# Kernel tuning notes

Hardware: AMD Instinct MI355X
Metric: run time of the kernel (lower is better)

## Reference

```python
import jax, jax.numpy as jnp
import numpy as np

W_BIT, OUT_F, IN_F, K = 4, 4096, 4096, 16
B, S = 4, 2048


def setup_inputs() -> dict:
    key = jax.random.key(0)
    k1, k2, k3, k4 = jax.random.split(key, 4)
    x = jax.random.normal(k1, (B, S, IN_F), dtype=jnp.float16)
    # bit-packed signs: 8 signs per byte, stored as int32 in [0, 256)
    qweight = jax.random.randint(k2, (W_BIT, OUT_F * IN_F // 8), 0, 256, dtype=jnp.int32)
    u = jax.random.normal(k3, (W_BIT, OUT_F, K), dtype=jnp.float16) * jnp.float16(0.1)
    vt = jax.random.normal(k4, (W_BIT, K, IN_F), dtype=jnp.float16) * jnp.float16(0.1)
    return {"x": x, "qweight": qweight, "u": u, "vt": vt}


def _unpack_sign(qweight, out_f, in_f, dtype):
    # [w_bit, N/8] packed bytes -> [w_bit, out_f, in_f] signs in {-1, +1}
    bits = (qweight[:, :, None] >> jnp.arange(8, dtype=qweight.dtype)) & 1
    sign = (2 * bits - 1).reshape(qweight.shape[0], out_f, in_f)
    return sign.astype(dtype)


def reference(x, qweight, u, vt):
    w_bit, out_f, _ = u.shape
    in_f = vt.shape[2]
    sign = _unpack_sign(qweight, out_f, in_f, u.dtype)          # [w_bit, out, in]
    lowrank = jnp.einsum('bok,bki->boi', u, vt)                  # per-bit u @ vt
    w = jnp.sum(sign * lowrank, axis=0)                          # [out, in]
    return x @ w.T                                               # [B, S, out]
```

## Files before the change

### kernel.cpp

```cpp
#include <hip/hip_runtime.h>
#include <stdint.h>


#define W_BITS 4
#define OUT_F  4096
#define IN_F   4096
#define K_RANK 16
#define M_TOT  8192
#define QW_PER_BIT (OUT_F * IN_F / 8)

typedef __attribute__((ext_vector_type(8))) short bf16x8;
typedef __attribute__((ext_vector_type(4))) float f32x4;

__device__ __forceinline__ unsigned short f2bf(float f) {
  union { float f; unsigned int u; } c; c.f = f;
  unsigned int r = c.u + 0x7fffu + ((c.u >> 16) & 1u);
  return (unsigned short)(r >> 16);
}

__global__ __launch_bounds__(256) void convert_x(
    const float* __restrict__ X, unsigned short* __restrict__ Xb, int n8)
{
  const int stride = gridDim.x * blockDim.x;
  for (int i = blockIdx.x * blockDim.x + threadIdx.x; i < n8; i += stride) {
    const f32x4 a = *reinterpret_cast<const f32x4*>(X + (size_t)i * 8);
    const f32x4 b = *reinterpret_cast<const f32x4*>(X + (size_t)i * 8 + 4);
    unsigned short o8[8] = {f2bf(a[0]), f2bf(a[1]), f2bf(a[2]), f2bf(a[3]),
                            f2bf(b[0]), f2bf(b[1]), f2bf(b[2]), f2bf(b[3])};
    *reinterpret_cast<uint4*>(Xb + (size_t)i * 8) = *reinterpret_cast<const uint4*>(o8);
  }
}

#define TO 4

__global__ __launch_bounds__(256) void build_w(
    const int*   __restrict__ qw,
    const float* __restrict__ u,
    const float* __restrict__ vt,
    unsigned short* __restrict__ w)
{
  const int tid = blockIdx.x * 256 + threadIdx.x;
  const int ig  = tid & 511;
  const int i0  = ig << 3;
  const int ob  = (tid >> 9) << 2;

  float acc[TO][8];
  #pragma unroll
  for (int t = 0; t < TO; ++t)
    #pragma unroll
    for (int ii = 0; ii < 8; ++ii) acc[t][ii] = 0.0f;

  #pragma unroll
  for (int bit = 0; bit < W_BITS; ++bit) {
    float lr[TO][8];
    #pragma unroll
    for (int t = 0; t < TO; ++t)
      #pragma unroll
      for (int ii = 0; ii < 8; ++ii) lr[t][ii] = 0.0f;

    const float* vbase = vt + (size_t)(bit * K_RANK) * IN_F + i0;
    const float* ubase = u + (size_t)(bit * OUT_F + ob) * K_RANK;

    #pragma unroll
    for (int k = 0; k < K_RANK; ++k) {
      const f32x4 v0 = *reinterpret_cast<const f32x4*>(vbase + (size_t)k * IN_F);
      const f32x4 v1 = *reinterpret_cast<const f32x4*>(vbase + (size_t)k * IN_F + 4);
      float vf[8] = {v0[0], v0[1], v0[2], v0[3], v1[0], v1[1], v1[2], v1[3]};
      #pragma unroll
      for (int t = 0; t < TO; ++t) {
        const float uk = ubase[t * K_RANK + k];
        #pragma unroll
        for (int ii = 0; ii < 8; ++ii) lr[t][ii] += uk * vf[ii];
      }
    }

    #pragma unroll
    for (int t = 0; t < TO; ++t) {
      const int q = qw[(size_t)bit * QW_PER_BIT + (size_t)(ob + t) * (IN_F / 8) + ig];
      #pragma unroll
      for (int ii = 0; ii < 8; ++ii)
        acc[t][ii] += ((q >> ii) & 1) ? lr[t][ii] : -lr[t][ii];
    }
  }

  #pragma unroll
  for (int t = 0; t < TO; ++t) {
    unsigned short o8[8];
    #pragma unroll
    for (int ii = 0; ii < 8; ++ii) o8[ii] = f2bf(acc[t][ii]);
    *reinterpret_cast<uint4*>(w + (size_t)(ob + t) * IN_F + i0) =
        *reinterpret_cast<const uint4*>(o8);
  }
}

__device__ __forceinline__ void gll16(unsigned short* lds, const unsigned short* g) {
  __builtin_amdgcn_global_load_lds(
      (const __attribute__((address_space(1))) unsigned int*)g,
      (__attribute__((address_space(3))) unsigned int*)lds,
      16, 0, 0);
}

__global__ __launch_bounds__(512, 2) void gemm_256(
    const unsigned short* __restrict__ X,
    const unsigned short* __restrict__ W,
    float* __restrict__ out)
{
  __shared__ __align__(16) unsigned short Al[2][256][64];
  __shared__ __align__(16) unsigned short Bl[2][256][64];

  const int bid = blockIdx.x;
  const int swz = (bid & 7) * 64 + (bid >> 3);
  const int bm = swz >> 4;
  const int bn = swz & 15;

  const int tid  = threadIdx.x;
  const int lane = tid & 63;
  const int wid  = tid >> 6;
  const int wm   = wid >> 2;
  const int wn   = wid & 3;

  const int sr = tid >> 3;
  const int sc = (((tid & 7) ^ (sr & 7)) << 3);

  const unsigned short* Abase = X + (size_t)(bm * 256 + sr) * IN_F + sc;
  const unsigned short* Bbase = W + (size_t)(bn * 256 + sr) * IN_F + sc;
  unsigned short* Alt = &Al[0][0][0] + tid * 8;
  unsigned short* Blt = &Bl[0][0][0] + tid * 8;

  const int fr  = lane & 15;
  const int sw0 = (((lane >> 4) ^ (fr & 7)) << 3);
  const int aRow = (wm * 16 + fr) * 64;
  const int bRow = (wn * 16 + fr) * 64;
  const unsigned short* Ar = &Al[0][0][0];
  const unsigned short* Br = &Bl[0][0][0];

  f32x4 acc[8][4];
  #pragma unroll
  for (int f = 0; f < 8; ++f)
    #pragma unroll
    for (int g = 0; g < 4; ++g)
      acc[f][g] = (f32x4){0.f, 0.f, 0.f, 0.f};

#define STAGE(buf, h, tn_) do {                                                        \
    const unsigned short* gs_ = ((h) < 2 ? Abase : Bbase)                              \
        + (size_t)(((h) & 1) * 128) * IN_F + (size_t)(tn_) * 64;                       \
    unsigned short* ld_ = ((h) < 2 ? Alt : Blt) + (buf) * 16384 + ((h) & 1) * 8192;    \
    gll16(ld_, gs_);                                                                   \
    gll16(ld_ + 4096, gs_ + (size_t)64 * IN_F);                                        \
  } while (0)

#define WAITBAR() do {                                                                 \
    asm volatile("s_waitcnt vmcnt(4)" ::: "memory");                                   \
    __builtin_amdgcn_s_barrier();                                                      \
    __builtin_amdgcn_sched_barrier(0);                                                 \
  } while (0)

#define PH_READ_A(mh_) {                                                               \
    _Pragma("unroll") for (int f = 0; f < 4; ++f)                                      \
      _Pragma("unroll") for (int ks = 0; ks < 2; ++ks)                                 \
        aF[f][ks] = *reinterpret_cast<const bf16x8*>(                                  \
            Ar + cbase + ((mh_) * 4 + f) * 2048 + aRow + ((ks * 32) ^ sw0)); }

#define PH_READ_B(nh_, dst_) {                                                         \
    _Pragma("unroll") for (int g = 0; g < 2; ++g)                                      \
      _Pragma("unroll") for (int ks = 0; ks < 2; ++ks)                                 \
        dst_[g][ks] = *reinterpret_cast<const bf16x8*>(                                \
            Br + cbase + ((nh_) * 2 + g) * 4096 + bRow + ((ks * 32) ^ sw0)); }

#define PH_MFMA(mh_, nh_, bsrc_) do {                                                  \
    __builtin_amdgcn_s_setprio(1);                                                     \
    _Pragma("unroll") for (int f = 0; f < 4; ++f)                                      \
      _Pragma("unroll") for (int g = 0; g < 2; ++g)                                    \
        _Pragma("unroll") for (int ks = 0; ks < 2; ++ks)                               \
          acc[(mh_) * 4 + f][(nh_) * 2 + g] = __builtin_amdgcn_mfma_f32_16x16x32_bf16( \
              aF[f][ks], bsrc_[g][ks], acc[(mh_) * 4 + f][(nh_) * 2 + g], 0, 0, 0);    \
    __builtin_amdgcn_s_setprio(0);                                                     \
  } while (0)

  STAGE(0, 0, 0);
  STAGE(0, 2, 0);
  STAGE(0, 3, 0);
  STAGE(0, 1, 0);
  asm volatile("s_waitcnt vmcnt(4)" ::: "memory");
  __builtin_amdgcn_s_barrier();
  __builtin_amdgcn_sched_barrier(0);

  bf16x8 aF[4][2], bF0[2][2], bF1[2][2];

  #pragma unroll 2
  for (int T = 0; T < 64; ++T) {
    const int cc = T & 1, oo = cc ^ 1;
    const int tn = (T < 63) ? T + 1 : 63;
    const int cbase = cc * 16384;

    PH_READ_A(0); PH_READ_B(0, bF0);
    STAGE(oo, 0, tn);
    WAITBAR();
    PH_MFMA(0, 0, bF0);
    __builtin_amdgcn_s_barrier();

    PH_READ_B(1, bF1);
    STAGE(oo, 2, tn);
    WAITBAR();
    PH_MFMA(0, 1, bF1);
    __builtin_amdgcn_s_barrier();

    PH_READ_A(1);
    STAGE(oo, 3, tn);
    WAITBAR();
    PH_MFMA(1, 1, bF1);
    __builtin_amdgcn_s_barrier();

    STAGE(oo, 1, tn);
    WAITBAR();
    PH_MFMA(1, 0, bF0);
    __builtin_amdgcn_s_barrier();
  }

  asm volatile("s_waitcnt vmcnt(0)" ::: "memory");

  const int rsub = (lane >> 4) << 2;
  #pragma unroll
  for (int f = 0; f < 8; ++f) {
    const int row = bm * 256 + (f * 2 + wm) * 16 + rsub;
    #pragma unroll
    for (int g = 0; g < 4; ++g) {
      const int col = bn * 256 + (g * 4 + wn) * 16 + (lane & 15);
      float* op = out + (size_t)row * OUT_F + col;
      #pragma unroll
      for (int j = 0; j < 4; ++j) op[(size_t)j * OUT_F] = acc[f][g][j];
    }
  }
#undef STAGE
#undef WAITBAR
#undef PH_READ_A
#undef PH_READ_B
#undef PH_MFMA
}

#define BM 128
#define BN 128
#define BK 32

__device__ __forceinline__ uint4 cvt8(f32x4 a, f32x4 b) {
  unsigned short o8[8] = {f2bf(a[0]), f2bf(a[1]), f2bf(a[2]), f2bf(a[3]),
                          f2bf(b[0]), f2bf(b[1]), f2bf(b[2]), f2bf(b[3])};
  return *reinterpret_cast<const uint4*>(o8);
}

__global__ __launch_bounds__(256) void gemm_f32stage(
    const float* __restrict__ X,
    const unsigned short* __restrict__ W,
    float* __restrict__ out)
{
  __shared__ __align__(16) unsigned short As[BM * BK];
  __shared__ __align__(16) unsigned short Bs[BN * BK];

  const int nbn = OUT_F / BN;
  const int cpx = (M_TOT / BM) * nbn / 8;
  const int bid = blockIdx.x;
  const int swz = (bid & 7) * cpx + (bid >> 3);
  const int bm = swz / nbn;
  const int bn = swz % nbn;

  const int tid  = threadIdx.x;
  const int lane = tid & 63;
  const int wid  = tid >> 6;
  const int wm   = wid >> 1;
  const int wn   = wid & 1;
  const int srow = tid >> 2;
  const int scol = (tid & 3) << 3;

  const float*          Ag = X + (size_t)(bm * BM + srow) * IN_F + scol;
  const unsigned short* Bg = W + (size_t)(bn * BN + srow) * IN_F + scol;

  const int fr = lane & 15;
  const int fk = (lane >> 4) << 3;

  f32x4 acc[4][4];
  #pragma unroll
  for (int m = 0; m < 4; ++m)
    #pragma unroll
    for (int n = 0; n < 4; ++n)
      acc[m][n] = (f32x4){0.f, 0.f, 0.f, 0.f};

  for (int k0 = 0; k0 < IN_F; k0 += BK) {
    const f32x4 a0a = *reinterpret_cast<const f32x4*>(Ag + k0);
    const f32x4 a0b = *reinterpret_cast<const f32x4*>(Ag + k0 + 4);
    const f32x4 a1a = *reinterpret_cast<const f32x4*>(Ag + (size_t)64 * IN_F + k0);
    const f32x4 a1b = *reinterpret_cast<const f32x4*>(Ag + (size_t)64 * IN_F + k0 + 4);
    const uint4 b0  = *reinterpret_cast<const uint4*>(Bg + k0);
    const uint4 b1  = *reinterpret_cast<const uint4*>(Bg + (size_t)64 * IN_F + k0);

    __syncthreads();
    *reinterpret_cast<uint4*>(As + tid * 8)        = cvt8(a0a, a0b);
    *reinterpret_cast<uint4*>(As + 2048 + tid * 8) = cvt8(a1a, a1b);
    *reinterpret_cast<uint4*>(Bs + tid * 8)        = b0;
    *reinterpret_cast<uint4*>(Bs + 2048 + tid * 8) = b1;
    __syncthreads();

    bf16x8 af[4], bfv[4];
    #pragma unroll
    for (int m = 0; m < 4; ++m)
      af[m] = *reinterpret_cast<const bf16x8*>(&As[(wm * 64 + m * 16 + fr) * BK + fk]);
    #pragma unroll
    for (int n = 0; n < 4; ++n)
      bfv[n] = *reinterpret_cast<const bf16x8*>(&Bs[(wn * 64 + n * 16 + fr) * BK + fk]);

    #pragma unroll
    for (int m = 0; m < 4; ++m)
      #pragma unroll
      for (int n = 0; n < 4; ++n)
        acc[m][n] = __builtin_amdgcn_mfma_f32_16x16x32_bf16(af[m], bfv[n], acc[m][n], 0, 0, 0);
  }

  const int rsub = (lane >> 4) << 2;
  #pragma unroll
  for (int m = 0; m < 4; ++m) {
    #pragma unroll
    for (int n = 0; n < 4; ++n) {
      const int col = bn * BN + wn * 64 + n * 16 + (lane & 15);
      #pragma unroll
      for (int j = 0; j < 4; ++j) {
        const int row = bm * BM + wm * 64 + m * 16 + rsub + j;
        out[(size_t)row * OUT_F + col] = acc[m][n][j];
      }
    }
  }
}

extern "C" void kernel_launch(void* const* d_in, const int* in_sizes, int n_in,
                              void* d_out, int out_size, void* d_ws, size_t ws_size,
                              hipStream_t stream) {
  (void)in_sizes; (void)n_in; (void)out_size;

  const float* x  = (const float*)d_in[0];
  const int*   qw = (const int*)d_in[1];
  const float* u  = (const float*)d_in[2];
  const float* vt = (const float*)d_in[3];
  float* out = (float*)d_out;

  unsigned short* w = (unsigned short*)d_ws;
  const size_t W_BYTES  = (size_t)OUT_F * IN_F * 2;
  const size_t XB_BYTES = (size_t)M_TOT * IN_F * 2;

  build_w<<<dim3(2048), dim3(256), 0, stream>>>(qw, u, vt, w);

  if (ws_size >= W_BYTES + XB_BYTES) {
    unsigned short* xb = w + (size_t)OUT_F * IN_F;
    convert_x<<<dim3(2048), dim3(256), 0, stream>>>(x, xb, M_TOT * IN_F / 8);
    gemm_256<<<dim3(512), dim3(512), 0, stream>>>(xb, w, out);
  } else {
    gemm_f32stage<<<dim3(2048), dim3(256), 0, stream>>>(x, w, out);
  }
}
```

Baseline: 365.7 us.

## Interleave LDS fragment reads with MFMAs in software-pipelined GEMM main loop

Restructures the bf16 GEMM main loop so LDS fragment reads for the next phase, and for the next K-tile, are issued between MFMA groups instead of in separate read phases before compute. Manual sched_barriers and explicit lgkmcnt waits control the ordering, and A/B fragments for the first tile are preloaded before the loop. The loop is unrolled by two with swapped register roles. This aims to hide LDS latency behind matrix-core work, at the cost of tighter hand scheduling and possible register pressure or hazards on buffer reuse.

```diff
diff --git a/kernel.cpp b/kernel.cpp
--- a/kernel.cpp
+++ b/kernel.cpp
@@ -155,26 +155,80 @@
     __builtin_amdgcn_sched_barrier(0);                                                 \
   } while (0)
 
-#define PH_READ_A(mh_) {                                                               \
-    _Pragma("unroll") for (int f = 0; f < 4; ++f)                                      \
-      _Pragma("unroll") for (int ks = 0; ks < 2; ++ks)                                 \
-        aF[f][ks] = *reinterpret_cast<const bf16x8*>(                                  \
-            Ar + cbase + ((mh_) * 4 + f) * 2048 + aRow + ((ks * 32) ^ sw0)); }
-
-#define PH_READ_B(nh_, dst_) {                                                         \
-    _Pragma("unroll") for (int g = 0; g < 2; ++g)                                      \
-      _Pragma("unroll") for (int ks = 0; ks < 2; ++ks)                                 \
-        dst_[g][ks] = *reinterpret_cast<const bf16x8*>(                                \
-            Br + cbase + ((nh_) * 2 + g) * 4096 + bRow + ((ks * 32) ^ sw0)); }
-
-#define PH_MFMA(mh_, nh_, bsrc_) do {                                                  \
+#define LGKMW(n_) do {                                                                 \
+    asm volatile("s_waitcnt lgkmcnt(" #n_ ")" ::: "memory");                           \
+    __builtin_amdgcn_sched_barrier(0);                                                 \
+  } while (0)
+
+#define SB() __builtin_amdgcn_sched_barrier(0)
+
+#define ENDPH() do {                                                                   \
+    __builtin_amdgcn_sched_barrier(0);                                                 \
+    __builtin_amdgcn_s_barrier();                                                      \
+  } while (0)
+
+#define RD_A(base_, mh_, f_, ks_)                                                      \
+    aF[f_][ks_] = *reinterpret_cast<const bf16x8*>(                                    \
+        Ar + (base_) + ((mh_) * 4 + (f_)) * 2048 + aRow + (((ks_) * 32) ^ sw0))
+
+#define RD_B(dst_, base_, nh_, g_, ks_)                                                \
+    dst_[g_][ks_] = *reinterpret_cast<const bf16x8*>(                                  \
+        Br + (base_) + ((nh_) * 2 + (g_)) * 4096 + bRow + (((ks_) * 32) ^ sw0))
+
+#define MF(mh_, nh_, f_, g_, ks_, bsrc_)                                               \
+    acc[(mh_) * 4 + (f_)][(nh_) * 2 + (g_)] = __builtin_amdgcn_mfma_f32_16x16x32_bf16( \
+        aF[f_][ks_], bsrc_[g_][ks_], acc[(mh_) * 4 + (f_)][(nh_) * 2 + (g_)], 0, 0, 0)
+
+#define MF4(mh_, nh_, f_, bsrc_) do {                                                  \
+    MF(mh_, nh_, f_, 0, 0, bsrc_); MF(mh_, nh_, f_, 0, 1, bsrc_);                      \
+    MF(mh_, nh_, f_, 1, 0, bsrc_); MF(mh_, nh_, f_, 1, 1, bsrc_); } while (0)
+
+#define KTILE(P_, Q_, CC_, OO_, tn_) do {                                              \
+    const int cb_ = (CC_) * 16384, ob_ = (OO_) * 16384;                                \
+                       \
+    STAGE(OO_, 2, tn_);                                                                \
+    WAITBAR();                                                                         \
+    LGKMW(0);                                                                          \
     __builtin_amdgcn_s_setprio(1);                                                     \
-    _Pragma("unroll") for (int f = 0; f < 4; ++f)                                      \
-      _Pragma("unroll") for (int g = 0; g < 2; ++g)                                    \
-        _Pragma("unroll") for (int ks = 0; ks < 2; ++ks)                               \
-          acc[(mh_) * 4 + f][(nh_) * 2 + g] = __builtin_amdgcn_mfma_f32_16x16x32_bf16( \
-              aF[f][ks], bsrc_[g][ks], acc[(mh_) * 4 + f][(nh_) * 2 + g], 0, 0, 0);    \
+    RD_B(Q_, cb_, 1, 0, 0); SB(); MF4(0, 0, 0, P_); SB();                              \
+    RD_B(Q_, cb_, 1, 0, 1); SB(); MF4(0, 0, 1, P_); SB();                              \
+    RD_B(Q_, cb_, 1, 1, 0); SB(); MF4(0, 0, 2, P_); SB();                              \
+    RD_B(Q_, cb_, 1, 1, 1); SB(); MF4(0, 0, 3, P_);                                    \
     __builtin_amdgcn_s_setprio(0);                                                     \
+    ENDPH();                                                                           \
+                        \
+    STAGE(OO_, 0, tn_);                                                                \
+    WAITBAR();                                                                         \
+    LGKMW(0);                                                                          \
+    __builtin_amdgcn_s_setprio(1);                                                     \
+    MF4(0, 1, 0, Q_); SB(); RD_A(cb_, 1, 0, 0); RD_A(cb_, 1, 0, 1); SB();              \
+    MF4(0, 1, 1, Q_); SB(); RD_A(cb_, 1, 1, 0); RD_A(cb_, 1, 1, 1); SB();              \
+    MF4(0, 1, 2, Q_); SB(); RD_A(cb_, 1, 2, 0); RD_A(cb_, 1, 2, 1); SB();              \
+    MF4(0, 1, 3, Q_); SB(); RD_A(cb_, 1, 3, 0); RD_A(cb_, 1, 3, 1);                    \
+    __builtin_amdgcn_s_setprio(0);                                                     \
+    ENDPH();                                                                           \
+                \
+    STAGE(OO_, 3, tn_);                                                                \
+    WAITBAR();                                                                         \
+    LGKMW(0);                                                                          \
+    __builtin_amdgcn_s_setprio(1);                                                     \
+    MF4(1, 1, 0, Q_); MF4(1, 1, 1, Q_); MF4(1, 1, 2, Q_); MF4(1, 1, 3, Q_);            \
+    __builtin_amdgcn_s_setprio(0);                                                     \
+    SB();                                                                              \
+    RD_B(Q_, ob_, 0, 0, 0); RD_B(Q_, ob_, 0, 0, 1);                                    \
+    RD_B(Q_, ob_, 0, 1, 0); RD_B(Q_, ob_, 0, 1, 1);                                    \
+    ENDPH();                                                                           \
+                  \
+    STAGE(OO_, 1, tn_);                                                                \
+    WAITBAR();                                                                         \
+    LGKMW(4);                                                                          \
+    __builtin_amdgcn_s_setprio(1);                                                     \
+    MF4(1, 0, 0, P_); SB(); RD_A(ob_, 0, 0, 0); RD_A(ob_, 0, 0, 1); SB();              \
+    MF4(1, 0, 1, P_); SB(); RD_A(ob_, 0, 1, 0); RD_A(ob_, 0, 1, 1); SB();              \
+    MF4(1, 0, 2, P_); SB(); RD_A(ob_, 0, 2, 0); RD_A(ob_, 0, 2, 1); SB();              \
+    MF4(1, 0, 3, P_); SB(); RD_A(ob_, 0, 3, 0); RD_A(ob_, 0, 3, 1);                    \
+    __builtin_amdgcn_s_setprio(0);                                                     \
+    ENDPH();                                                                           \
   } while (0)
 
   STAGE(0, 0, 0);
@@ -186,38 +240,23 @@
   __builtin_amdgcn_sched_barrier(0);
 
   bf16x8 aF[4][2], bF0[2][2], bF1[2][2];
-
-  #pragma unroll 2
-  for (int T = 0; T < 64; ++T) {
-    const int cc = T & 1, oo = cc ^ 1;
-    const int tn = (T < 63) ? T + 1 : 63;
-    const int cbase = cc * 16384;
-
-    PH_READ_A(0); PH_READ_B(0, bF0);
-    STAGE(oo, 0, tn);
-    WAITBAR();
-    PH_MFMA(0, 0, bF0);
-    __builtin_amdgcn_s_barrier();
-
-    PH_READ_B(1, bF1);
-    STAGE(oo, 2, tn);
-    WAITBAR();
-    PH_MFMA(0, 1, bF1);
-    __builtin_amdgcn_s_barrier();
-
-    PH_READ_A(1);
-    STAGE(oo, 3, tn);
-    WAITBAR();
-    PH_MFMA(1, 1, bF1);
-    __builtin_amdgcn_s_barrier();
-
-    STAGE(oo, 1, tn);
-    WAITBAR();
-    PH_MFMA(1, 0, bF0);
-    __builtin_amdgcn_s_barrier();
-  }
-
-  asm volatile("s_waitcnt vmcnt(0)" ::: "memory");
+  RD_A(0, 0, 0, 0); RD_A(0, 0, 0, 1);
+  RD_A(0, 0, 1, 0); RD_A(0, 0, 1, 1);
+  RD_A(0, 0, 2, 0); RD_A(0, 0, 2, 1);
+  RD_A(0, 0, 3, 0); RD_A(0, 0, 3, 1);
+  RD_B(bF0, 0, 0, 0, 0); RD_B(bF0, 0, 0, 0, 1);
+  RD_B(bF0, 0, 0, 1, 0); RD_B(bF0, 0, 0, 1, 1);
+
+  #pragma unroll 1
+  for (int Th = 0; Th < 32; ++Th) {
+    const int T0 = 2 * Th;
+    const int tnA = T0 + 1;
+    const int tnB = (T0 + 2 < 64) ? T0 + 2 : 63;
+    KTILE(bF0, bF1, 0, 1, tnA);
+    KTILE(bF1, bF0, 1, 0, tnB);
+  }
+
+  asm volatile("s_waitcnt vmcnt(0) lgkmcnt(0)" ::: "memory");
 
   const int rsub = (lane >> 4) << 2;
   #pragma unroll
@@ -233,9 +272,14 @@
   }
 #undef STAGE
 #undef WAITBAR
-#undef PH_READ_A
-#undef PH_READ_B
-#undef PH_MFMA
+#undef LGKMW
+#undef SB
+#undef ENDPH
+#undef RD_A
+#undef RD_B
+#undef MF
+#undef MF4
+#undef KTILE
 }
 
 #define BM 128
```

Result: no change. 367.6 us (+0.5%).

## Restructure GEMM main loop to one barrier per tile with batched LDS reads

Applied to the files above, without the earlier changes.

The bf16 GEMM K-loop is rescheduled. Each iteration now waits for all global-to-LDS loads and does a single barrier, then issues all four staging loads for the next tile up front. LDS fragment reads are batched and gated by lgkmcnt waits instead of four barrier-separated phases. This cuts barrier count and lets LDS reads overlap MFMAs, but the full vmcnt(0) wait at the start of each iteration may expose more global-load latency than the old partial vmcnt(4) waits.

```diff
diff --git a/kernel.cpp b/kernel.cpp
--- a/kernel.cpp
+++ b/kernel.cpp
@@ -149,31 +149,35 @@
     gll16(ld_ + 4096, gs_ + (size_t)64 * IN_F);                                        \
   } while (0)
 
-#define WAITBAR() do {                                                                 \
-    asm volatile("s_waitcnt vmcnt(4)" ::: "memory");                                   \
-    __builtin_amdgcn_s_barrier();                                                      \
+#define LGKMW(n_) do {                                                                 \
+    asm volatile("s_waitcnt lgkmcnt(" #n_ ")" ::: "memory");                           \
     __builtin_amdgcn_sched_barrier(0);                                                 \
   } while (0)
 
-#define PH_READ_A(mh_) {                                                               \
-    _Pragma("unroll") for (int f = 0; f < 4; ++f)                                      \
-      _Pragma("unroll") for (int ks = 0; ks < 2; ++ks)                                 \
-        aF[f][ks] = *reinterpret_cast<const bf16x8*>(                                  \
-            Ar + cbase + ((mh_) * 4 + f) * 2048 + aRow + ((ks * 32) ^ sw0)); }
-
-#define PH_READ_B(nh_, dst_) {                                                         \
-    _Pragma("unroll") for (int g = 0; g < 2; ++g)                                      \
-      _Pragma("unroll") for (int ks = 0; ks < 2; ++ks)                                 \
-        dst_[g][ks] = *reinterpret_cast<const bf16x8*>(                                \
-            Br + cbase + ((nh_) * 2 + g) * 4096 + bRow + ((ks * 32) ^ sw0)); }
-
-#define PH_MFMA(mh_, nh_, bsrc_) do {                                                  \
+#define SB() __builtin_amdgcn_sched_barrier(0)
+
+#define RD_A(base_, mh_, f_, ks_)                                                      \
+    aF[f_][ks_] = *reinterpret_cast<const bf16x8*>(                                    \
+        Ar + (base_) + ((mh_) * 4 + (f_)) * 2048 + aRow + (((ks_) * 32) ^ sw0))
+
+#define RD_B(dst_, base_, nh_, g_, ks_)                                                \
+    dst_[g_][ks_] = *reinterpret_cast<const bf16x8*>(                                  \
+        Br + (base_) + ((nh_) * 2 + (g_)) * 4096 + bRow + (((ks_) * 32) ^ sw0))
+
+#define MF(mh_, nh_, f_, g_, ks_, bsrc_)                                               \
+    acc[(mh_) * 4 + (f_)][(nh_) * 2 + (g_)] = __builtin_amdgcn_mfma_f32_16x16x32_bf16( \
+        aF[f_][ks_], bsrc_[g_][ks_], acc[(mh_) * 4 + (f_)][(nh_) * 2 + (g_)], 0, 0, 0)
+
+#define MF16(mh_, nh_, bsrc_) do {                                                     \
     __builtin_amdgcn_s_setprio(1);                                                     \
-    _Pragma("unroll") for (int f = 0; f < 4; ++f)                                      \
-      _Pragma("unroll") for (int g = 0; g < 2; ++g)                                    \
-        _Pragma("unroll") for (int ks = 0; ks < 2; ++ks)                               \
-          acc[(mh_) * 4 + f][(nh_) * 2 + g] = __builtin_amdgcn_mfma_f32_16x16x32_bf16( \
-              aF[f][ks], bsrc_[g][ks], acc[(mh_) * 4 + f][(nh_) * 2 + g], 0, 0, 0);    \
+    MF(mh_, nh_, 0, 0, 0, bsrc_); MF(mh_, nh_, 0, 0, 1, bsrc_);                        \
+    MF(mh_, nh_, 0, 1, 0, bsrc_); MF(mh_, nh_, 0, 1, 1, bsrc_);                        \
+    MF(mh_, nh_, 1, 0, 0, bsrc_); MF(mh_, nh_, 1, 0, 1, bsrc_);                        \
+    MF(mh_, nh_, 1, 1, 0, bsrc_); MF(mh_, nh_, 1, 1, 1, bsrc_);                        \
+    MF(mh_, nh_, 2, 0, 0, bsrc_); MF(mh_, nh_, 2, 0, 1, bsrc_);                        \
+    MF(mh_, nh_, 2, 1, 0, bsrc_); MF(mh_, nh_, 2, 1, 1, bsrc_);                        \
+    MF(mh_, nh_, 3, 0, 0, bsrc_); MF(mh_, nh_, 3, 0, 1, bsrc_);                        \
+    MF(mh_, nh_, 3, 1, 0, bsrc_); MF(mh_, nh_, 3, 1, 1, bsrc_);                        \
     __builtin_amdgcn_s_setprio(0);                                                     \
   } while (0)
 
@@ -181,9 +185,6 @@
   STAGE(0, 2, 0);
   STAGE(0, 3, 0);
   STAGE(0, 1, 0);
-  asm volatile("s_waitcnt vmcnt(4)" ::: "memory");
-  __builtin_amdgcn_s_barrier();
-  __builtin_amdgcn_sched_barrier(0);
 
   bf16x8 aF[4][2], bF0[2][2], bF1[2][2];
 
@@ -191,33 +192,45 @@
   for (int T = 0; T < 64; ++T) {
     const int cc = T & 1, oo = cc ^ 1;
     const int tn = (T < 63) ? T + 1 : 63;
-    const int cbase = cc * 16384;
-
-    PH_READ_A(0); PH_READ_B(0, bF0);
+    const int cb = cc * 16384;
+
+    asm volatile("s_waitcnt vmcnt(0)" ::: "memory");
+    __builtin_amdgcn_s_barrier();
+    __builtin_amdgcn_sched_barrier(0);
+
     STAGE(oo, 0, tn);
-    WAITBAR();
-    PH_MFMA(0, 0, bF0);
-    __builtin_amdgcn_s_barrier();
-
-    PH_READ_B(1, bF1);
     STAGE(oo, 2, tn);
-    WAITBAR();
-    PH_MFMA(0, 1, bF1);
-    __builtin_amdgcn_s_barrier();
-
-    PH_READ_A(1);
     STAGE(oo, 3, tn);
-    WAITBAR();
-    PH_MFMA(1, 1, bF1);
-    __builtin_amdgcn_s_barrier();
-
     STAGE(oo, 1, tn);
-    WAITBAR();
-    PH_MFMA(1, 0, bF0);
-    __builtin_amdgcn_s_barrier();
-  }
-
-  asm volatile("s_waitcnt vmcnt(0)" ::: "memory");
+    SB();
+
+    RD_A(cb, 0, 0, 0); RD_A(cb, 0, 0, 1); RD_A(cb, 0, 1, 0); RD_A(cb, 0, 1, 1);
+    RD_A(cb, 0, 2, 0); RD_A(cb, 0, 2, 1); RD_A(cb, 0, 3, 0); RD_A(cb, 0, 3, 1);
+    SB();
+    RD_B(bF0, cb, 0, 0, 0); RD_B(bF0, cb, 0, 0, 1);
+    RD_B(bF0, cb, 0, 1, 0); RD_B(bF0, cb, 0, 1, 1);
+    SB();
+    RD_B(bF1, cb, 1, 0, 0); RD_B(bF1, cb, 1, 0, 1);
+    RD_B(bF1, cb, 1, 1, 0); RD_B(bF1, cb, 1, 1, 1);
+    SB();
+
+    LGKMW(4);
+    MF16(0, 0, bF0);
+
+    LGKMW(0);
+    MF16(0, 1, bF1);
+    SB();
+
+    RD_A(cb, 1, 0, 0); RD_A(cb, 1, 0, 1); RD_A(cb, 1, 1, 0); RD_A(cb, 1, 1, 1);
+    RD_A(cb, 1, 2, 0); RD_A(cb, 1, 2, 1); RD_A(cb, 1, 3, 0); RD_A(cb, 1, 3, 1);
+    SB();
+
+    LGKMW(0);
+    MF16(1, 1, bF1);
+    MF16(1, 0, bF0);
+  }
+
+  asm volatile("s_waitcnt vmcnt(0) lgkmcnt(0)" ::: "memory");
 
   const int rsub = (lane >> 4) << 2;
   #pragma unroll
@@ -232,10 +245,12 @@
     }
   }
 #undef STAGE
-#undef WAITBAR
-#undef PH_READ_A
-#undef PH_READ_B
-#undef PH_MFMA
+#undef LGKMW
+#undef SB
+#undef RD_A
+#undef RD_B
+#undef MF
+#undef MF16
 }
 
 #define BM 128
```

Measured after the change: 366.2 us. About the same (+0.1%).
